# Kernel optimization log

Measured on AMD Instinct MI355X. Metric: run time of the kernel, lower is better.

Reference implementation:

```python
import jax, jax.numpy as jnp
import numpy as np

B, S, D = 4, 2048, 1024
E, TOP_K = 8, 2
CAPACITY_FACTOR = 1.1
H = 4 * D  # expert hidden dim


def setup_inputs() -> dict:
    key = jax.random.key(0)
    ks = jax.random.split(key, 12)
    sc = 0.02
    return {
        "x": jax.random.normal(ks[0], (B, S, D), jnp.float32),
        "noise": jax.random.normal(ks[1], (B, S, E), jnp.float32),
        "W_route": jax.random.normal(ks[2], (D, E), jnp.float32) * sc,
        "b_route": jnp.zeros((E,), jnp.float32),
        "W_noise": jax.random.normal(ks[3], (D, E), jnp.float32) * sc,
        "b_noise": jnp.zeros((E,), jnp.float32),
        "W1": jax.random.normal(ks[4], (E, D, H), jnp.float32) * sc,
        "b1": jnp.zeros((E, H), jnp.float32),
        "W2": jax.random.normal(ks[5], (E, H, D), jnp.float32) * sc,
        "b2": jnp.zeros((E, D), jnp.float32),
    }


def reference(x, noise, W_route, b_route, W_noise, b_noise, W1, b1, W2, b2):
    # ---- NoisyTopkRouter ----
    logits = x @ W_route + b_route                  # [B,S,E]
    noise_logits = x @ W_noise + b_noise            # [B,S,E]
    noisy = logits + noise * jax.nn.softplus(noise_logits)
    top_vals, top_idx = jax.lax.top_k(noisy, TOP_K)  # [B,S,k]
    probs_k = jax.nn.softmax(top_vals, axis=-1)      # softmax over sparse(-inf elsewhere) == softmax over top-k
    onehot = jax.nn.one_hot(top_idx, E, dtype=x.dtype)          # [B,S,k,E]
    router_probs = jnp.einsum('bske,bsk->bse', onehot, probs_k)  # [B,S,E]
    expert_mask = onehot.sum(axis=-2)                            # [B,S,E] (top_k indices are distinct)
    lb_loss = E * jnp.sum(router_probs.mean(axis=(0, 1)) * expert_mask.mean(axis=(0, 1)))

    # ---- capacity-limited dispatch / expert MLP / combine ----
    T = B * S
    cap = int(T * TOP_K / E * CAPACITY_FACTOR)
    flat_x = x.reshape(T, D)
    flat_gate = router_probs.reshape(T, E)
    mask = expert_mask.reshape(T, E) > 0                         # token selects expert
    pos = jnp.cumsum(mask.astype(jnp.int32), axis=0)             # 1-based slot within expert
    keep = mask & (pos <= cap)                                   # first `cap` tokens per expert (flat order)
    priority = jnp.where(keep, jnp.arange(T)[:, None], T)        # [T,E]
    order = jnp.argsort(priority, axis=0)[:cap]                  # [cap,E] token ids (stable: token order)
    valid = (jnp.take_along_axis(priority, order, axis=0) < T).T  # [E,cap]
    gather_idx = order.T                                         # [E,cap]

    x_e = flat_x[gather_idx]                                     # [E,cap,D]
    h = jax.nn.relu(jnp.einsum('ecd,edh->ech', x_e, W1) + b1[:, None, :])
    out_e = jnp.einsum('ech,ehd->ecd', h, W2) + b2[:, None, :]   # dropout is identity in eval mode
    gate = flat_gate[gather_idx, jnp.arange(E)[:, None]]         # [E,cap]
    weighted = out_e * (gate * valid)[..., None]
    updates = jnp.zeros_like(flat_x).at[gather_idx.reshape(-1)].add(weighted.reshape(-1, D))
    return updates.reshape(B, S, D), lb_loss
```

## Files before the change

### kernel.cpp

```cpp
#include <hip/hip_runtime.h>
#include <hip/hip_bf16.h>

#define D_DIM 1024
#define H_DIM 4096
#define E_NUM 8
#define T_TOK 8192
#define CAPN 2252
#define CAP_PAD 2304
#define MT 9

typedef __attribute__((ext_vector_type(8))) short short8;
typedef __attribute__((ext_vector_type(4))) float f32x4;
typedef const __attribute__((address_space(1))) void* gas_ptr;
typedef __attribute__((address_space(3))) void* las_ptr;

__device__ __forceinline__ unsigned short f2bf(float f) {
    __hip_bfloat16 h = __float2bfloat16(f);
    return __builtin_bit_cast(unsigned short, h);
}

__global__ void router_kernel(const float* __restrict__ x,
                              const float* __restrict__ noise,
                              const float* __restrict__ Wr,
                              const float* __restrict__ br,
                              const float* __restrict__ Wn,
                              const float* __restrict__ bn,
                              __hip_bfloat16* __restrict__ xb,
                              int* __restrict__ tok_e,
                              float* __restrict__ tok_g)
{
    const int l = threadIdx.x & 63;
    const int w = threadIdx.x >> 6;
    const int t = blockIdx.x * 4 + w;
    const float* xr = x + (size_t)t * D_DIM;

    float ar[8] = {0,0,0,0,0,0,0,0};
    float an[8] = {0,0,0,0,0,0,0,0};
#pragma unroll
    for (int i = 0; i < 4; ++i) {
        int d = i * 256 + l * 4;
        float4 xv = *(const float4*)(xr + d);
        ushort4 xq;
        xq.x = f2bf(xv.x); xq.y = f2bf(xv.y); xq.z = f2bf(xv.z); xq.w = f2bf(xv.w);
        *(ushort4*)(xb + (size_t)t * D_DIM + d) = xq;
        float xs[4] = {xv.x, xv.y, xv.z, xv.w};
#pragma unroll
        for (int j = 0; j < 4; ++j) {
            const float* wrp = Wr + (size_t)(d + j) * 8;
            float4 wa = *(const float4*)wrp;
            float4 wb = *(const float4*)(wrp + 4);
            ar[0] = fmaf(xs[j], wa.x, ar[0]); ar[1] = fmaf(xs[j], wa.y, ar[1]);
            ar[2] = fmaf(xs[j], wa.z, ar[2]); ar[3] = fmaf(xs[j], wa.w, ar[3]);
            ar[4] = fmaf(xs[j], wb.x, ar[4]); ar[5] = fmaf(xs[j], wb.y, ar[5]);
            ar[6] = fmaf(xs[j], wb.z, ar[6]); ar[7] = fmaf(xs[j], wb.w, ar[7]);
            const float* wnp = Wn + (size_t)(d + j) * 8;
            float4 na = *(const float4*)wnp;
            float4 nb = *(const float4*)(wnp + 4);
            an[0] = fmaf(xs[j], na.x, an[0]); an[1] = fmaf(xs[j], na.y, an[1]);
            an[2] = fmaf(xs[j], na.z, an[2]); an[3] = fmaf(xs[j], na.w, an[3]);
            an[4] = fmaf(xs[j], nb.x, an[4]); an[5] = fmaf(xs[j], nb.y, an[5]);
            an[6] = fmaf(xs[j], nb.z, an[6]); an[7] = fmaf(xs[j], nb.w, an[7]);
        }
    }
#pragma unroll
    for (int e = 0; e < 8; ++e) {
#pragma unroll
        for (int s = 32; s > 0; s >>= 1) {
            ar[e] += __shfl_xor(ar[e], s, 64);
            an[e] += __shfl_xor(an[e], s, 64);
        }
    }
    if (l == 0) {
        float nv[8];
#pragma unroll
        for (int e = 0; e < 8; ++e) {
            float z = an[e] + bn[e];
            float sp = fmaxf(z, 0.f) + log1pf(expf(-fabsf(z)));
            nv[e] = ar[e] + br[e] + noise[(size_t)t * 8 + e] * sp;
        }
        int e0 = 0; float v0 = nv[0];
#pragma unroll
        for (int e = 1; e < 8; ++e) if (nv[e] > v0) { v0 = nv[e]; e0 = e; }
        int e1 = -1; float v1 = -3.4e38f;
#pragma unroll
        for (int e = 0; e < 8; ++e) if (e != e0 && nv[e] > v1) { v1 = nv[e]; e1 = e; }
        float ex = expf(v1 - v0);
        float p0 = 1.f / (1.f + ex);
        float p1 = ex * p0;
        tok_e[2 * t]     = e0; tok_e[2 * t + 1] = e1;
        tok_g[2 * t]     = p0; tok_g[2 * t + 1] = p1;
    }
}

__global__ void scan_kernel(const int* __restrict__ tok_e,
                            const float* __restrict__ tok_g,
                            int* __restrict__ routed,
                            int* __restrict__ inv,
                            int* __restrict__ nkept,
                            float* __restrict__ lb_out)
{
    const int e = threadIdx.x >> 6;
    const int l = threadIdx.x & 63;
    __shared__ float s_g[E_NUM];
    __shared__ int   s_c[E_NUM];

    int run = 0;
    float gsum = 0.f;
    for (int b = 0; b < 8; ++b) {
        int2  ev[16];
        float2 gv[16];
#pragma unroll
        for (int c = 0; c < 16; ++c) {
            int t = (b * 16 + c) * 64 + l;
            ev[c] = ((const int2*)tok_e)[t];
            gv[c] = ((const float2*)tok_g)[t];
        }
#pragma unroll
        for (int c = 0; c < 16; ++c) {
            int t = (b * 16 + c) * 64 + l;
            int j = (ev[c].x == e) ? 0 : ((ev[c].y == e) ? 1 : -1);
            bool sel = (j >= 0);
            unsigned long long m = __ballot(sel);
            if (sel) {
                int pos = run + __popcll(m & ((1ull << l) - 1ull));
                if (pos < CAPN) {
                    routed[e * CAP_PAD + pos] = t;
                    inv[2 * t + j] = e * CAP_PAD + pos;
                }
                gsum += (j == 0) ? gv[c].x : gv[c].y;
            }
            run += __popcll(m);
        }
    }
#pragma unroll
    for (int s = 32; s > 0; s >>= 1) gsum += __shfl_xor(gsum, s, 64);
    int nk = min(run, CAPN);
    for (int s = nk + l; s < CAP_PAD; s += 64) routed[e * CAP_PAD + s] = 0;
    if (l == 0) { nkept[e] = nk; s_g[e] = gsum; s_c[e] = run; }
    __syncthreads();
    if (threadIdx.x == 0) {
        float lb = 0.f;
        for (int ee = 0; ee < E_NUM; ++ee)
            lb += (s_g[ee] / (float)T_TOK) * ((float)s_c[ee] / (float)T_TOK);
        lb_out[0] = lb * (float)E_NUM;
    }
}

__global__ void gather_kernel(const ushort* __restrict__ xb,
                              const int* __restrict__ routed,
                              ushort* __restrict__ xg)
{
    const int dc = blockIdx.x & 127;
    const int e  = blockIdx.x >> 7;
    ushort* dst = xg + (size_t)(e * 128 + dc) * CAP_PAD * 8;
    const int* rte = routed + e * CAP_PAD;
#pragma unroll
    for (int p = 0; p < 9; ++p) {
        int m = p * 256 + threadIdx.x;
        int tok = rte[m];
        ulonglong2 v = *(const ulonglong2*)(xb + (size_t)tok * D_DIM + dc * 8);
        *(ulonglong2*)(dst + (size_t)m * 8) = v;
    }
}

__global__ void chunk_weights(const float* __restrict__ in,
                              ushort* __restrict__ out,
                              int K, int N)
{
    __shared__ float tile[64][65];
    const int e = blockIdx.z;
    const int k0 = blockIdx.y * 64, n0 = blockIdx.x * 64;
    const float* src = in + (size_t)e * K * N;
    ushort* dst = out + (size_t)e * (K / 8) * N * 8;
    const int t = threadIdx.x;
    const int rr = t >> 4, c4 = (t & 15) * 4;
#pragma unroll
    for (int p = 0; p < 4; ++p) {
        int r = p * 16 + rr;
        float4 v = *(const float4*)(src + (size_t)(k0 + r) * N + n0 + c4);
        tile[r][c4]     = v.x; tile[r][c4 + 1] = v.y;
        tile[r][c4 + 2] = v.z; tile[r][c4 + 3] = v.w;
    }
    __syncthreads();
    const int n = t & 63, kc = t >> 6;
#pragma unroll
    for (int p = 0; p < 2; ++p) {
        int kcc = p * 4 + kc;
        ushort g[8];
#pragma unroll
        for (int j = 0; j < 8; ++j) g[j] = f2bf(tile[kcc * 8 + j][n]);
        *(short8*)(dst + ((size_t)(k0 / 8 + kcc) * N + n0 + n) * 8) = *(const short8*)g;
    }
}

template <int MODE>
__global__ __launch_bounds__(512, 2) void ffn_gemm(
    const ushort* __restrict__ A,
    const ushort* __restrict__ Bt,
    const float* __restrict__ bias,
    const int* __restrict__ nkept,
    ushort* __restrict__ outH,
    float*  __restrict__ outP,
    int sshift, int nkt)
{
    constexpr int KD = (MODE == 1) ? D_DIM : H_DIM;
    constexpr int ND = (MODE == 1) ? H_DIM : D_DIM;
    constexpr int NC = KD / 8;
    __shared__ ushort lds[65536];

    unsigned total = gridDim.x * gridDim.y * gridDim.z;
    unsigned flat  = blockIdx.x + gridDim.x * (blockIdx.y + gridDim.y * blockIdx.z);
    unsigned sw    = (flat & 7) * (total >> 3) + (flat >> 3);
    unsigned bn    = sw % gridDim.x;
    unsigned t1    = sw / gridDim.x;
    unsigned bm    = t1 % gridDim.y;
    unsigned bz    = t1 / gridDim.y;

    const int e  = (int)(bz >> sshift);
    const int sp = (int)(bz & ((1u << sshift) - 1u));
    const int m0 = (int)bm * 256, n0 = (int)bn * 256;
    if (m0 >= nkept[e]) return;
    const int kc0 = sp * (nkt << 2);

    const int tid  = threadIdx.x;
    const int lane = tid & 63;
    const int w    = tid >> 6;
    const int ra   = tid & 255;
    const int chi  = tid >> 8;
    const int wq   = (w & 3) * 1024;

    const ushort* Ae = A  + ((size_t)e * NC * CAP_PAD + (size_t)(m0 + ra)) * 8;
    const ushort* Be = Bt + ((size_t)e * NC * ND + (size_t)(n0 + ra)) * 8;
    const size_t sAc = (size_t)CAP_PAD * 8;
    const size_t sBc = (size_t)ND * 8;

    auto stage_A = [&](int ktI, int stB) {
        int ac = kc0 + (ktI << 2);
        __builtin_amdgcn_global_load_lds((gas_ptr)(Ae + (size_t)(ac + chi) * sAc),
            (las_ptr)((char*)lds + stB + chi * 4096 + wq), 16, 0, 0);
        __builtin_amdgcn_global_load_lds((gas_ptr)(Ae + (size_t)(ac + 2 + chi) * sAc),
            (las_ptr)((char*)lds + stB + (2 + chi) * 4096 + wq), 16, 0, 0);
    };
    auto stage_B = [&](int ktI, int stB) {
        int ac = kc0 + (ktI << 2);
        __builtin_amdgcn_global_load_lds((gas_ptr)(Be + (size_t)(ac + chi) * sBc),
            (las_ptr)((char*)lds + stB + 16384 + chi * 4096 + wq), 16, 0, 0);
        __builtin_amdgcn_global_load_lds((gas_ptr)(Be + (size_t)(ac + 2 + chi) * sBc),
            (las_ptr)((char*)lds + stB + 16384 + (2 + chi) * 4096 + wq), 16, 0, 0);
    };

    stage_A(0, 0);      stage_B(0, 0);
    stage_A(1, 32768);  stage_B(1, 32768);
    stage_A(2, 65536);  stage_B(2, 65536);
    asm volatile("s_waitcnt vmcnt(8)" ::: "memory");
    __builtin_amdgcn_s_barrier();

    f32x4 acc[8][4] = {};
    const int wm = (w >> 2) * 128;
    const int wn = (w & 3) * 64;
    const int fr = lane & 15;
    const int fq = lane >> 4;

    for (int kt = 0; kt < nkt; ++kt) {
        const ushort* Ard = lds + (kt & 3) * 16384;
        const ushort* Brd = Ard + 8192;

        short8 bfr[4], af[8];
#pragma unroll
        for (int j = 0; j < 4; ++j)
            bfr[j] = *(const short8*)(Brd + fq * 2048 + (wn + j * 16 + fr) * 8);
#pragma unroll
        for (int i = 0; i < 8; ++i)
            af[i] = *(const short8*)(Ard + fq * 2048 + (wm + i * 16 + fr) * 8);

        const int ktp = min(kt + 3, nkt - 1);
        const int wst = ((kt + 3) & 3) * 32768;
        stage_A(ktp, wst);
        stage_B(ktp, wst);

        __builtin_amdgcn_s_setprio(1);
#pragma unroll
        for (int i = 0; i < 8; ++i)
#pragma unroll
            for (int j = 0; j < 4; ++j)
                acc[i][j] = __builtin_amdgcn_mfma_f32_16x16x32_bf16(af[i], bfr[j], acc[i][j], 0, 0, 0);
        __builtin_amdgcn_s_setprio(0);

        asm volatile("s_waitcnt vmcnt(8)" ::: "memory");
        __builtin_amdgcn_s_barrier();
    }

#pragma unroll
    for (int j = 0; j < 4; ++j) {
        int nc = n0 + wn + j * 16 + fr;
        float bv = (MODE == 1) ? bias[e * ND + nc] : 0.f;
#pragma unroll
        for (int i = 0; i < 8; ++i) {
            int mr = m0 + wm + i * 16 + (fq << 2);
#pragma unroll
            for (int r = 0; r < 4; ++r) {
                float v = acc[i][j][r] + bv;
                if (MODE == 1) {
                    v = fmaxf(v, 0.f);
                    outH[(((size_t)e * 512 + (nc >> 3)) * CAP_PAD + mr + r) * 8 + (nc & 7)] = f2bf(v);
                } else {
                    outP[((size_t)(sp * E_NUM + e) * CAP_PAD + mr + r) * D_DIM + nc] = v;
                }
            }
        }
    }
}

__global__ void combine_kernel(const float* __restrict__ part,
                               const int* __restrict__ inv,
                               const float* __restrict__ tok_g,
                               const float* __restrict__ b2,
                               int S,
                               float* __restrict__ out)
{
    const int t = blockIdx.x;
    const int d = threadIdx.x * 4;
    float4 r = make_float4(0.f, 0.f, 0.f, 0.f);
#pragma unroll
    for (int j = 0; j < 2; ++j) {
        int i = inv[2 * t + j];
        if (i >= 0) {
            float g = tok_g[2 * t + j];
            int e = i / CAP_PAD;
            float4 a = *(const float4*)(b2 + (size_t)e * D_DIM + d);
            for (int s = 0; s < S; ++s) {
                float4 p = *(const float4*)(part + ((size_t)s * E_NUM * CAP_PAD + i) * D_DIM + d);
                a.x += p.x; a.y += p.y; a.z += p.z; a.w += p.w;
            }
            r.x = fmaf(g, a.x, r.x); r.y = fmaf(g, a.y, r.y);
            r.z = fmaf(g, a.z, r.z); r.w = fmaf(g, a.w, r.w);
        }
    }
    *(float4*)(out + (size_t)t * D_DIM + d) = r;
}

extern "C" void kernel_launch(void* const* d_in, const int* in_sizes, int n_in,
                              void* d_out, int out_size, void* d_ws, size_t ws_size,
                              hipStream_t stream)
{
    const float* x  = (const float*)d_in[0];
    const float* nz = (const float*)d_in[1];
    const float* Wr = (const float*)d_in[2];
    const float* br = (const float*)d_in[3];
    const float* Wn = (const float*)d_in[4];
    const float* bn = (const float*)d_in[5];
    const float* W1 = (const float*)d_in[6];
    const float* b1 = (const float*)d_in[7];
    const float* W2 = (const float*)d_in[8];
    const float* b2 = (const float*)d_in[9];
    float* out = (float*)d_out;
    char* ws = (char*)d_ws;

    const size_t sz_w2c = (size_t)E_NUM * (H_DIM / 8) * D_DIM * 8 * 2;
    const size_t sz_h   = (size_t)E_NUM * 512 * CAP_PAD * 8 * 2;
    const size_t o_w2c  = 0;
    const size_t o_h    = o_w2c + sz_w2c;
    const size_t o_sm   = o_h + sz_h;
    const size_t o_dyn  = o_sm + (1u << 20);
    const size_t sz_xg  = (size_t)E_NUM * 128 * CAP_PAD * 8 * 2;
    const size_t sz_xb  = (size_t)T_TOK * D_DIM * 2;
    const size_t sz_w1c = (size_t)E_NUM * (D_DIM / 8) * H_DIM * 8 * 2;
    const size_t sz_p1  = sz_xg + sz_xb + sz_w1c;
    const size_t sz_part1 = (size_t)E_NUM * CAP_PAD * D_DIM * 4;

    int sshift = 1;
    while (sshift > 0) {
        size_t need = o_dyn + ((sz_part1 << sshift) > sz_p1 ? (sz_part1 << sshift) : sz_p1);
        if (need <= ws_size) break;
        --sshift;
    }
    const int S = 1 << sshift;

    ushort* w2c  = (ushort*)(ws + o_w2c);
    ushort* hbuf = (ushort*)(ws + o_h);
    int*    rt   = (int*)(ws + o_sm);
    int*    te   = (int*)(ws + o_sm + 131072);
    float*  tg   = (float*)(ws + o_sm + 262144);
    int*    inv  = (int*)(ws + o_sm + 393216);
    int*    nk   = (int*)(ws + o_sm + 524288);
    ushort* xg   = (ushort*)(ws + o_dyn);
    ushort* xb   = (ushort*)(ws + o_dyn + sz_xg);
    ushort* w1c  = (ushort*)(ws + o_dyn + sz_xg + sz_xb);
    float*  part = (float*)(ws + o_dyn);

    hipMemsetAsync(inv, 0xFF, (size_t)T_TOK * 2 * 4, stream);

    router_kernel<<<T_TOK / 4, 256, 0, stream>>>(x, nz, Wr, br, Wn, bn,
                                                 (__hip_bfloat16*)xb, te, tg);
    scan_kernel<<<1, 512, 0, stream>>>(te, tg, rt, inv, nk, out + (size_t)T_TOK * D_DIM);
    chunk_weights<<<dim3(H_DIM / 64, D_DIM / 64, E_NUM), 256, 0, stream>>>(W1, w1c, D_DIM, H_DIM);
    chunk_weights<<<dim3(D_DIM / 64, H_DIM / 64, E_NUM), 256, 0, stream>>>(W2, w2c, H_DIM, D_DIM);
    gather_kernel<<<E_NUM * 128, 256, 0, stream>>>(xb, rt, xg);

    ffn_gemm<1><<<dim3(H_DIM / 256, MT, E_NUM), 512, 0, stream>>>(
        xg, w1c, b1, nk, hbuf, nullptr, 0, D_DIM / 32);

    ffn_gemm<2><<<dim3(D_DIM / 256, MT, E_NUM << sshift), 512, 0, stream>>>(
        hbuf, w2c, nullptr, nk, nullptr, part, sshift, (H_DIM / 32) >> sshift);

    combine_kernel<<<T_TOK, 256, 0, stream>>>(part, inv, tg, b2, S, out);
}
```

Before: 612.0 us.

## Switch FFN GEMM to double-buffered K=64 tiles with interleaved load/compute phases

The expert GEMM main loop moves from a 4-stage ring of K=32 tiles to a 2-stage double buffer of K=64 tiles. Each K-tile is split into four compute quarters, and the global-to-LDS loads for the next tile are issued a quarter at a time between them, with barriers in between. This cuts the loop trip count in half and overlaps prefetch with MFMA work at finer granularity, and it holds fewer A-fragment registers at once. The cost is prefetch depth dropping from three tiles to one and roughly four barriers per iteration instead of one, which can expose more memory latency.

```diff
diff --git a/kernel.cpp b/kernel.cpp
--- a/kernel.cpp
+++ b/kernel.cpp
@@ -220,7 +220,7 @@
     const int sp = (int)(bz & ((1u << sshift) - 1u));
     const int m0 = (int)bm * 256, n0 = (int)bn * 256;
     if (m0 >= nkept[e]) return;
-    const int kc0 = sp * (nkt << 2);
+    const int kc0 = sp * (nkt << 3);
 
     const int tid  = threadIdx.x;
     const int lane = tid & 63;
@@ -234,25 +234,23 @@
     const size_t sAc = (size_t)CAP_PAD * 8;
     const size_t sBc = (size_t)ND * 8;
 
-    auto stage_A = [&](int ktI, int stB) {
-        int ac = kc0 + (ktI << 2);
-        __builtin_amdgcn_global_load_lds((gas_ptr)(Ae + (size_t)(ac + chi) * sAc),
-            (las_ptr)((char*)lds + stB + chi * 4096 + wq), 16, 0, 0);
-        __builtin_amdgcn_global_load_lds((gas_ptr)(Ae + (size_t)(ac + 2 + chi) * sAc),
-            (las_ptr)((char*)lds + stB + (2 + chi) * 4096 + wq), 16, 0, 0);
+    auto issueA = [&](int ktI, int stB, int c4) {
+        int cb = kc0 + (ktI << 3) + c4;
+        __builtin_amdgcn_global_load_lds((gas_ptr)(Ae + (size_t)(cb + chi) * sAc),
+            (las_ptr)((char*)lds + stB + (c4 + chi) * 4096 + wq), 16, 0, 0);
+        __builtin_amdgcn_global_load_lds((gas_ptr)(Ae + (size_t)(cb + 2 + chi) * sAc),
+            (las_ptr)((char*)lds + stB + (c4 + 2 + chi) * 4096 + wq), 16, 0, 0);
     };
-    auto stage_B = [&](int ktI, int stB) {
-        int ac = kc0 + (ktI << 2);
-        __builtin_amdgcn_global_load_lds((gas_ptr)(Be + (size_t)(ac + chi) * sBc),
-            (las_ptr)((char*)lds + stB + 16384 + chi * 4096 + wq), 16, 0, 0);
-        __builtin_amdgcn_global_load_lds((gas_ptr)(Be + (size_t)(ac + 2 + chi) * sBc),
-            (las_ptr)((char*)lds + stB + 16384 + (2 + chi) * 4096 + wq), 16, 0, 0);
+    auto issueB = [&](int ktI, int stB, int c4) {
+        int cb = kc0 + (ktI << 3) + c4;
+        __builtin_amdgcn_global_load_lds((gas_ptr)(Be + (size_t)(cb + chi) * sBc),
+            (las_ptr)((char*)lds + stB + 32768 + (c4 + chi) * 4096 + wq), 16, 0, 0);
+        __builtin_amdgcn_global_load_lds((gas_ptr)(Be + (size_t)(cb + 2 + chi) * sBc),
+            (las_ptr)((char*)lds + stB + 32768 + (c4 + 2 + chi) * 4096 + wq), 16, 0, 0);
     };
 
-    stage_A(0, 0);      stage_B(0, 0);
-    stage_A(1, 32768);  stage_B(1, 32768);
-    stage_A(2, 65536);  stage_B(2, 65536);
-    asm volatile("s_waitcnt vmcnt(8)" ::: "memory");
+    issueA(0, 0, 0); issueB(0, 0, 0); issueA(0, 0, 4); issueB(0, 0, 4);
+    asm volatile("s_waitcnt vmcnt(0)" ::: "memory");
     __builtin_amdgcn_s_barrier();
 
     f32x4 acc[8][4] = {};
@@ -261,32 +259,76 @@
     const int fr = lane & 15;
     const int fq = lane >> 4;
 
+    short8 af[4], bfr[4];
     for (int kt = 0; kt < nkt; ++kt) {
-        const ushort* Ard = lds + (kt & 3) * 16384;
-        const ushort* Brd = Ard + 8192;
-
-        short8 bfr[4], af[8];
+        const int b = kt & 1;
+        const ushort* Ard = lds + b * 32768;
+        const ushort* Brd = Ard + 16384;
+        const int ktn = min(kt + 1, nkt - 1);
+        const int wrB = (b ^ 1) * 65536;
+
 #pragma unroll
         for (int j = 0; j < 4; ++j)
             bfr[j] = *(const short8*)(Brd + fq * 2048 + (wn + j * 16 + fr) * 8);
 #pragma unroll
-        for (int i = 0; i < 8; ++i)
+        for (int i = 0; i < 4; ++i)
             af[i] = *(const short8*)(Ard + fq * 2048 + (wm + i * 16 + fr) * 8);
-
-        const int ktp = min(kt + 3, nkt - 1);
-        const int wst = ((kt + 3) & 3) * 32768;
-        stage_A(ktp, wst);
-        stage_B(ktp, wst);
-
+        issueA(ktn, wrB, 0);
+        __builtin_amdgcn_s_barrier();
         __builtin_amdgcn_s_setprio(1);
 #pragma unroll
-        for (int i = 0; i < 8; ++i)
+        for (int i = 0; i < 4; ++i)
 #pragma unroll
             for (int j = 0; j < 4; ++j)
                 acc[i][j] = __builtin_amdgcn_mfma_f32_16x16x32_bf16(af[i], bfr[j], acc[i][j], 0, 0, 0);
         __builtin_amdgcn_s_setprio(0);
-
-        asm volatile("s_waitcnt vmcnt(8)" ::: "memory");
+        __builtin_amdgcn_s_barrier();
+
+#pragma unroll
+        for (int i = 0; i < 4; ++i)
+            af[i] = *(const short8*)(Ard + fq * 2048 + (wm + 64 + i * 16 + fr) * 8);
+        issueB(ktn, wrB, 0);
+        __builtin_amdgcn_s_barrier();
+        __builtin_amdgcn_s_setprio(1);
+#pragma unroll
+        for (int i = 0; i < 4; ++i)
+#pragma unroll
+            for (int j = 0; j < 4; ++j)
+                acc[4 + i][j] = __builtin_amdgcn_mfma_f32_16x16x32_bf16(af[i], bfr[j], acc[4 + i][j], 0, 0, 0);
+        __builtin_amdgcn_s_setprio(0);
+        asm volatile("s_waitcnt vmcnt(4)" ::: "memory");
+        __builtin_amdgcn_s_barrier();
+
+#pragma unroll
+        for (int j = 0; j < 4; ++j)
+            bfr[j] = *(const short8*)(Brd + 8192 + fq * 2048 + (wn + j * 16 + fr) * 8);
+#pragma unroll
+        for (int i = 0; i < 4; ++i)
+            af[i] = *(const short8*)(Ard + 8192 + fq * 2048 + (wm + i * 16 + fr) * 8);
+        issueA(ktn, wrB, 4);
+        __builtin_amdgcn_s_barrier();
+        __builtin_amdgcn_s_setprio(1);
+#pragma unroll
+        for (int i = 0; i < 4; ++i)
+#pragma unroll
+            for (int j = 0; j < 4; ++j)
+                acc[i][j] = __builtin_amdgcn_mfma_f32_16x16x32_bf16(af[i], bfr[j], acc[i][j], 0, 0, 0);
+        __builtin_amdgcn_s_setprio(0);
+        __builtin_amdgcn_s_barrier();
+
+#pragma unroll
+        for (int i = 0; i < 4; ++i)
+            af[i] = *(const short8*)(Ard + 8192 + fq * 2048 + (wm + 64 + i * 16 + fr) * 8);
+        issueB(ktn, wrB, 4);
+        __builtin_amdgcn_s_barrier();
+        __builtin_amdgcn_s_setprio(1);
+#pragma unroll
+        for (int i = 0; i < 4; ++i)
+#pragma unroll
+            for (int j = 0; j < 4; ++j)
+                acc[4 + i][j] = __builtin_amdgcn_mfma_f32_16x16x32_bf16(af[i], bfr[j], acc[4 + i][j], 0, 0, 0);
+        __builtin_amdgcn_s_setprio(0);
+        asm volatile("s_waitcnt vmcnt(4)" ::: "memory");
         __builtin_amdgcn_s_barrier();
     }
 
@@ -398,10 +440,10 @@
     gather_kernel<<<E_NUM * 128, 256, 0, stream>>>(xb, rt, xg);
 
     ffn_gemm<1><<<dim3(H_DIM / 256, MT, E_NUM), 512, 0, stream>>>(
-        xg, w1c, b1, nk, hbuf, nullptr, 0, D_DIM / 32);
+        xg, w1c, b1, nk, hbuf, nullptr, 0, D_DIM / 64);
 
     ffn_gemm<2><<<dim3(D_DIM / 256, MT, E_NUM << sshift), 512, 0, stream>>>(
-        hbuf, w2c, nullptr, nk, nullptr, part, sshift, (H_DIM / 32) >> sshift);
+        hbuf, w2c, nullptr, nk, nullptr, part, sshift, (H_DIM / 64) >> sshift);
 
     combine_kernel<<<T_TOK, 256, 0, stream>>>(part, inv, tg, b2, S, out);
 }
```

Measured after the change: 622.0 us. About the same (+1.6%).

## Shrink FFN GEMM tiles to 128x128 with 256-thread blocks and triple buffering

Applied to the files above, without the earlier changes.

Reworks the expert FFN GEMM from 256x256 tiles on 512-thread blocks with a four-stage LDS ring to 128x128 tiles on 256-thread blocks with a three-stage ring. It also reduces shared memory per block so that three blocks can be resident per CU. The aim is more blocks, better CU occupancy and less waste on partially filled capacity tiles. In exchange, arithmetic intensity per tile drops and global and L2 traffic rises, and prefetch runs only two stages ahead.

```diff
diff --git a/kernel.cpp b/kernel.cpp
--- a/kernel.cpp
+++ b/kernel.cpp
@@ -7,7 +7,7 @@
 #define T_TOK 8192
 #define CAPN 2252
 #define CAP_PAD 2304
-#define MT 9
+#define MT 18
 
 typedef __attribute__((ext_vector_type(8))) short short8;
 typedef __attribute__((ext_vector_type(4))) float f32x4;
@@ -194,7 +194,7 @@
 }
 
 template <int MODE>
-__global__ __launch_bounds__(512, 2) void ffn_gemm(
+__global__ __launch_bounds__(256, 3) void ffn_gemm(
     const ushort* __restrict__ A,
     const ushort* __restrict__ Bt,
     const float* __restrict__ bias,
@@ -206,7 +206,7 @@
     constexpr int KD = (MODE == 1) ? D_DIM : H_DIM;
     constexpr int ND = (MODE == 1) ? H_DIM : D_DIM;
     constexpr int NC = KD / 8;
-    __shared__ ushort lds[65536];
+    __shared__ ushort lds[24576];
 
     unsigned total = gridDim.x * gridDim.y * gridDim.z;
     unsigned flat  = blockIdx.x + gridDim.x * (blockIdx.y + gridDim.y * blockIdx.z);
@@ -218,76 +218,80 @@
 
     const int e  = (int)(bz >> sshift);
     const int sp = (int)(bz & ((1u << sshift) - 1u));
-    const int m0 = (int)bm * 256, n0 = (int)bn * 256;
+    const int m0 = (int)bm * 128, n0 = (int)bn * 128;
     if (m0 >= nkept[e]) return;
     const int kc0 = sp * (nkt << 2);
 
     const int tid  = threadIdx.x;
     const int lane = tid & 63;
     const int w    = tid >> 6;
-    const int ra   = tid & 255;
-    const int chi  = tid >> 8;
-    const int wq   = (w & 3) * 1024;
-
-    const ushort* Ae = A  + ((size_t)e * NC * CAP_PAD + (size_t)(m0 + ra)) * 8;
-    const ushort* Be = Bt + ((size_t)e * NC * ND + (size_t)(n0 + ra)) * 8;
+    const int chi  = w >> 1;
+    const int rhE  = (w & 1) * 64;
+    const int rhB  = (w & 1) * 1024;
+
+    const ushort* Ae = A  + ((size_t)e * NC * CAP_PAD + (size_t)(m0 + rhE + lane)) * 8;
+    const ushort* Be = Bt + ((size_t)e * NC * ND + (size_t)(n0 + rhE + lane)) * 8;
     const size_t sAc = (size_t)CAP_PAD * 8;
     const size_t sBc = (size_t)ND * 8;
 
-    auto stage_A = [&](int ktI, int stB) {
-        int ac = kc0 + (ktI << 2);
-        __builtin_amdgcn_global_load_lds((gas_ptr)(Ae + (size_t)(ac + chi) * sAc),
-            (las_ptr)((char*)lds + stB + chi * 4096 + wq), 16, 0, 0);
-        __builtin_amdgcn_global_load_lds((gas_ptr)(Ae + (size_t)(ac + 2 + chi) * sAc),
-            (las_ptr)((char*)lds + stB + (2 + chi) * 4096 + wq), 16, 0, 0);
+    auto issueA = [&](int ktI, int stB) {
+        int cb = kc0 + (ktI << 2);
+        __builtin_amdgcn_global_load_lds((gas_ptr)(Ae + (size_t)(cb + chi) * sAc),
+            (las_ptr)((char*)lds + stB + chi * 2048 + rhB), 16, 0, 0);
+        __builtin_amdgcn_global_load_lds((gas_ptr)(Ae + (size_t)(cb + 2 + chi) * sAc),
+            (las_ptr)((char*)lds + stB + (2 + chi) * 2048 + rhB), 16, 0, 0);
     };
-    auto stage_B = [&](int ktI, int stB) {
-        int ac = kc0 + (ktI << 2);
-        __builtin_amdgcn_global_load_lds((gas_ptr)(Be + (size_t)(ac + chi) * sBc),
-            (las_ptr)((char*)lds + stB + 16384 + chi * 4096 + wq), 16, 0, 0);
-        __builtin_amdgcn_global_load_lds((gas_ptr)(Be + (size_t)(ac + 2 + chi) * sBc),
-            (las_ptr)((char*)lds + stB + 16384 + (2 + chi) * 4096 + wq), 16, 0, 0);
+    auto issueB = [&](int ktI, int stB) {
+        int cb = kc0 + (ktI << 2);
+        __builtin_amdgcn_global_load_lds((gas_ptr)(Be + (size_t)(cb + chi) * sBc),
+            (las_ptr)((char*)lds + stB + 8192 + chi * 2048 + rhB), 16, 0, 0);
+        __builtin_amdgcn_global_load_lds((gas_ptr)(Be + (size_t)(cb + 2 + chi) * sBc),
+            (las_ptr)((char*)lds + stB + 8192 + (2 + chi) * 2048 + rhB), 16, 0, 0);
     };
 
-    stage_A(0, 0);      stage_B(0, 0);
-    stage_A(1, 32768);  stage_B(1, 32768);
-    stage_A(2, 65536);  stage_B(2, 65536);
-    asm volatile("s_waitcnt vmcnt(8)" ::: "memory");
+    issueA(0, 0);      issueB(0, 0);
+    issueA(1, 16384);  issueB(1, 16384);
+    asm volatile("s_waitcnt vmcnt(4)" ::: "memory");
     __builtin_amdgcn_s_barrier();
 
-    f32x4 acc[8][4] = {};
-    const int wm = (w >> 2) * 128;
-    const int wn = (w & 3) * 64;
+    f32x4 acc[4][4] = {};
+    const int wm = (w >> 1) * 64;
+    const int wn = (w & 1) * 64;
     const int fr = lane & 15;
     const int fq = lane >> 4;
 
+    int rdS = 0;
+    int wrB = 32768;
+
     for (int kt = 0; kt < nkt; ++kt) {
-        const ushort* Ard = lds + (kt & 3) * 16384;
-        const ushort* Brd = Ard + 8192;
-
-        short8 bfr[4], af[8];
+        const ushort* Ard = lds + rdS;
+        const ushort* Brd = Ard + 4096;
+
+        short8 af[4], bfr[4];
 #pragma unroll
         for (int j = 0; j < 4; ++j)
-            bfr[j] = *(const short8*)(Brd + fq * 2048 + (wn + j * 16 + fr) * 8);
-#pragma unroll
-        for (int i = 0; i < 8; ++i)
-            af[i] = *(const short8*)(Ard + fq * 2048 + (wm + i * 16 + fr) * 8);
-
-        const int ktp = min(kt + 3, nkt - 1);
-        const int wst = ((kt + 3) & 3) * 32768;
-        stage_A(ktp, wst);
-        stage_B(ktp, wst);
+            bfr[j] = *(const short8*)(Brd + fq * 1024 + (wn + j * 16 + fr) * 8);
+#pragma unroll
+        for (int i = 0; i < 4; ++i)
+            af[i] = *(const short8*)(Ard + fq * 1024 + (wm + i * 16 + fr) * 8);
+
+        const int ktp = min(kt + 2, nkt - 1);
+        issueA(ktp, wrB);
+        issueB(ktp, wrB);
 
         __builtin_amdgcn_s_setprio(1);
 #pragma unroll
-        for (int i = 0; i < 8; ++i)
+        for (int i = 0; i < 4; ++i)
 #pragma unroll
             for (int j = 0; j < 4; ++j)
                 acc[i][j] = __builtin_amdgcn_mfma_f32_16x16x32_bf16(af[i], bfr[j], acc[i][j], 0, 0, 0);
         __builtin_amdgcn_s_setprio(0);
 
-        asm volatile("s_waitcnt vmcnt(8)" ::: "memory");
+        asm volatile("s_waitcnt vmcnt(4)" ::: "memory");
         __builtin_amdgcn_s_barrier();
+
+        rdS = (rdS == 16384) ? 0 : rdS + 8192;
+        wrB = (wrB == 32768) ? 0 : wrB + 16384;
     }
 
 #pragma unroll
@@ -295,7 +299,7 @@
         int nc = n0 + wn + j * 16 + fr;
         float bv = (MODE == 1) ? bias[e * ND + nc] : 0.f;
 #pragma unroll
-        for (int i = 0; i < 8; ++i) {
+        for (int i = 0; i < 4; ++i) {
             int mr = m0 + wm + i * 16 + (fq << 2);
 #pragma unroll
             for (int r = 0; r < 4; ++r) {
@@ -397,10 +401,10 @@
     chunk_weights<<<dim3(D_DIM / 64, H_DIM / 64, E_NUM), 256, 0, stream>>>(W2, w2c, H_DIM, D_DIM);
     gather_kernel<<<E_NUM * 128, 256, 0, stream>>>(xb, rt, xg);
 
-    ffn_gemm<1><<<dim3(H_DIM / 256, MT, E_NUM), 512, 0, stream>>>(
+    ffn_gemm<1><<<dim3(H_DIM / 128, MT, E_NUM), 256, 0, stream>>>(
         xg, w1c, b1, nk, hbuf, nullptr, 0, D_DIM / 32);
 
-    ffn_gemm<2><<<dim3(D_DIM / 256, MT, E_NUM << sshift), 512, 0, stream>>>(
+    ffn_gemm<2><<<dim3(D_DIM / 128, MT, E_NUM << sshift), 256, 0, stream>>>(
         hbuf, w2c, nullptr, nk, nullptr, part, sshift, (H_DIM / 32) >> sshift);
 
     combine_kernel<<<T_TOK, 256, 0, stream>>>(part, inv, tg, b2, S, out);
```

Measured after the change: 604.9 us. Within noise of the previous version (-1.2%).
